# Performance work log

Hardware: AMD Instinct MI355X
Metric: run time of the kernel (lower is better)

The kernel has to match this reference:

```python
import jax, jax.numpy as jnp
import numpy as np
import math
from jax import lax

VOCAB = 32000
D = 128          # embedding_dim
S = 512          # seq_len == input_channels
B = 8
HID = 512        # hidden_size
NBUCK = 32       # n_buckets
NHYP = 5         # log2(n_buckets)
ENCODERS = 2
OUT = 6
EPS = 1e-5


def _positional_encoding(max_len, d):
    pos = np.arange(max_len, dtype=np.float32)[:, None]
    div = np.exp(np.arange(0, d, 2, dtype=np.float32) * (-math.log(10000.0) / d))
    pe = np.zeros((max_len, d), dtype=np.float32)
    pe[:, 0::2] = np.sin(pos * div)
    pe[:, 1::2] = np.cos(pos * div)
    return jnp.asarray(pe)


def setup_inputs() -> dict:
    key = jax.random.key(0)
    ks = jax.random.split(key, 10)
    emb = jax.random.normal(ks[0], (VOCAB, D), jnp.float32)
    emb = emb.at[VOCAB - 1].set(0.0)  # padding_idx row is zero in torch
    sc = 0.05
    return {
        "inputs": jax.random.randint(ks[1], (B, S), 0, VOCAB - 1),
        "emb": emb,
        # Faithful quirk: pe is indexed by x.size(0)=batch, so only pe[:B] is used.
        "pe": _positional_encoding(B, D),               # [B, D]
        "hyperplanes": jax.random.normal(ks[2], (D + 1, NHYP), jnp.float32),
        "Wq": jax.random.normal(ks[3], (D, D), jnp.float32) * sc,
        "bq": jnp.zeros((D,), jnp.float32),
        "Wv": jax.random.normal(ks[4], (D, D), jnp.float32) * sc,
        "bv": jnp.zeros((D,), jnp.float32),
        "ln_g": jnp.ones((D,), jnp.float32),
        "ln_b": jnp.zeros((D,), jnp.float32),
        "W1": jax.random.normal(ks[5], (D, HID), jnp.float32) * sc,
        "b1": jnp.zeros((HID,), jnp.float32),
        "W2": jax.random.normal(ks[6], (HID, D), jnp.float32) * sc,
        "b2": jnp.zeros((D,), jnp.float32),
        "Wm": jax.random.normal(ks[7], (S * D, OUT), jnp.float32) * 0.01,
        "bm": jnp.zeros((OUT,), jnp.float32),
    }


def _layernorm(x, g, b):
    mu = jnp.mean(x, axis=-1, keepdims=True)
    var = jnp.mean(jnp.square(x - mu), axis=-1, keepdims=True)
    return (x - mu) * lax.rsqrt(var + EPS) * g + b


def _lsh_attention(x, Wq, bq, Wv, bv, hyperplanes):
    q = x @ Wq + bq                                      # [B,S,D]
    v = x @ Wv + bv                                      # [B,S,D]
    # LSH bucket ids from q (hard threshold -> no grad through buckets)
    qh = jnp.concatenate([q, jnp.ones(q.shape[:-1] + (1,), q.dtype)], axis=-1)
    proj = jnp.einsum('bse,en->bsn', qh, hyperplanes)    # [B,S,NHYP]
    bits = (proj >= 0).astype(jnp.float32)
    pow2 = 2.0 ** jnp.arange(NHYP, dtype=jnp.float32)
    buckets = jnp.einsum('bsn,n->bs', bits, pow2).astype(jnp.int32)  # [B,S]
    scale = 1.0 / math.sqrt(D)

    def step(acc, i):
        # Faithful quirk: masked_fill zeros tokens IN bucket i (inverted mask).
        keep = (buckets != i)[..., None]                 # [B,S,1]
        qb = jnp.where(keep, q, 0.0)
        vb = jnp.where(keep, v, 0.0)
        att = jax.nn.softmax(jnp.einsum('bsd,btd->bst', qb, qb) * scale, axis=-1)
        return acc + jnp.einsum('bst,btd->bsd', att, vb), None

    out, _ = lax.scan(step, jnp.zeros_like(x), jnp.arange(NBUCK))
    return out


def reference(inputs, emb, pe, hyperplanes, Wq, bq, Wv, bv, ln_g, ln_b,
              W1, b1, W2, b2, Wm, bm):
    x = emb[inputs]                                      # [B,S,D]
    x = x + pe[:, None, :]                               # broadcast over seq (faithful quirk)
    for _ in range(ENCODERS):
        a = _lsh_attention(x, Wq, bq, Wv, bv, hyperplanes)
        x = _layernorm(a, ln_g, ln_b)
        x = (jax.nn.relu(x @ W1 + b1) @ W2 + b2) + x     # fc residual (dropout=eval)
        x = _layernorm(x, ln_g, ln_b)
    x = x.reshape(x.shape[0], -1)                        # [B, S*D]
    return x @ Wm + bm                                   # [B, OUT]
```

## Files before the change

kernel.cpp:

```cpp
#include <hip/hip_runtime.h>
#include <hip/hip_bf16.h>

#define BB   8
#define SS   512
#define DD   128
#define HH   512
#define NBK  32


__global__ void k_embed(const int* __restrict__ idx, const float* __restrict__ emb,
                        const float* __restrict__ pe, float* __restrict__ x) {
    int b = blockIdx.x;
    int t = b * 16384 + blockIdx.y * 256 + threadIdx.x;
    int tok = t >> 5, d4 = (t & 31) * 4;
    float4 ev = *(const float4*)&emb[(size_t)idx[tok] * DD + d4];
    float4 pv = *(const float4*)&pe[b * DD + d4];
    ev.x += pv.x; ev.y += pv.y; ev.z += pv.z; ev.w += pv.w;
    *(float4*)&x[(size_t)tok * DD + d4] = ev;
}

__global__ __launch_bounds__(256) void k_qvb(const float* __restrict__ x,
        const float* __restrict__ Wq, const float* __restrict__ bq,
        const float* __restrict__ Wv, const float* __restrict__ bv,
        const float* __restrict__ hyp,
        float* __restrict__ q, float* __restrict__ v, float* __restrict__ qT,
        int* __restrict__ bucket) {
    int rb = blockIdx.x * 32 + blockIdx.y;
    __shared__ __align__(16) float xs[16][132];
    __shared__ float qts[128][17];
    int tid = threadIdx.x;
    #pragma unroll
    for (int it = 0; it < 2; ++it) {
        int lin = tid + 256 * it;
        int r = lin >> 5, kq = (lin & 31) * 4;
        *(float4*)&xs[r][kq] = *(const float4*)&x[(size_t)(rb * 16 + r) * DD + kq];
    }
    __syncthreads();
    int tx = tid & 63;
    int ty = tid >> 6;
    float2 aq[4], av[4];
    #pragma unroll
    for (int i = 0; i < 4; ++i) { aq[i] = make_float2(0.f, 0.f); av[i] = make_float2(0.f, 0.f); }
    for (int g = 0; g < 32; ++g) {
        int kb = g * 4;
        float4 a0 = *(const float4*)&xs[ty * 4 + 0][kb];
        float4 a1 = *(const float4*)&xs[ty * 4 + 1][kb];
        float4 a2 = *(const float4*)&xs[ty * 4 + 2][kb];
        float4 a3 = *(const float4*)&xs[ty * 4 + 3][kb];
        #pragma unroll
        for (int j = 0; j < 4; ++j) {
            float2 wq = *(const float2*)&Wq[(size_t)(kb + j) * DD + tx * 2];
            float2 wv = *(const float2*)&Wv[(size_t)(kb + j) * DD + tx * 2];
            float c0 = (j == 0) ? a0.x : (j == 1) ? a0.y : (j == 2) ? a0.z : a0.w;
            float c1 = (j == 0) ? a1.x : (j == 1) ? a1.y : (j == 2) ? a1.z : a1.w;
            float c2 = (j == 0) ? a2.x : (j == 1) ? a2.y : (j == 2) ? a2.z : a2.w;
            float c3 = (j == 0) ? a3.x : (j == 1) ? a3.y : (j == 2) ? a3.z : a3.w;
            aq[0].x += c0 * wq.x; aq[0].y += c0 * wq.y; av[0].x += c0 * wv.x; av[0].y += c0 * wv.y;
            aq[1].x += c1 * wq.x; aq[1].y += c1 * wq.y; av[1].x += c1 * wv.x; av[1].y += c1 * wv.y;
            aq[2].x += c2 * wq.x; aq[2].y += c2 * wq.y; av[2].x += c2 * wv.x; av[2].y += c2 * wv.y;
            aq[3].x += c3 * wq.x; aq[3].y += c3 * wq.y; av[3].x += c3 * wv.x; av[3].y += c3 * wv.y;
        }
    }
    float2 bqv = *(const float2*)&bq[tx * 2];
    float2 bvv = *(const float2*)&bv[tx * 2];
    float2 oq[4], ov[4];
    #pragma unroll
    for (int i = 0; i < 4; ++i) {
        oq[i] = make_float2(aq[i].x + bqv.x, aq[i].y + bqv.y);
        ov[i] = make_float2(av[i].x + bvv.x, av[i].y + bvv.y);
        int row = rb * 16 + ty * 4 + i;
        *(float2*)&q[(size_t)row * DD + tx * 2] = oq[i];
        *(float2*)&v[(size_t)row * DD + tx * 2] = ov[i];
        qts[2 * tx][ty * 4 + i]     = oq[i].x;
        qts[2 * tx + 1][ty * 4 + i] = oq[i].y;
    }
    float h0[5], h1[5];
    #pragma unroll
    for (int h = 0; h < 5; ++h) {
        h0[h] = hyp[(2 * tx) * 5 + h];
        h1[h] = hyp[(2 * tx + 1) * 5 + h];
    }
    float pr[4][5];
    #pragma unroll
    for (int r = 0; r < 4; ++r)
        #pragma unroll
        for (int h = 0; h < 5; ++h)
            pr[r][h] = oq[r].x * h0[h] + oq[r].y * h1[h];
    #pragma unroll
    for (int o = 1; o < 64; o <<= 1)
        #pragma unroll
        for (int r = 0; r < 4; ++r)
            #pragma unroll
            for (int h = 0; h < 5; ++h)
                pr[r][h] += __shfl_xor(pr[r][h], o, 64);
    if (tx == 0) {
        #pragma unroll
        for (int r = 0; r < 4; ++r) {
            int bb = 0;
            #pragma unroll
            for (int h = 0; h < 5; ++h)
                if (pr[r][h] + hyp[128 * 5 + h] >= 0.f) bb |= (1 << h);
            bucket[rb * 16 + ty * 4 + r] = bb;
        }
    }
    __syncthreads();
    {
        int b  = blockIdx.x;
        int t0 = blockIdx.y * 16;
        int k  = tid >> 1, o = (tid & 1) * 8;
        float4 v0 = make_float4(qts[k][o], qts[k][o + 1], qts[k][o + 2], qts[k][o + 3]);
        float4 v1 = make_float4(qts[k][o + 4], qts[k][o + 5], qts[k][o + 6], qts[k][o + 7]);
        size_t base = ((size_t)b * DD + k) * SS + t0 + o;
        *(float4*)&qT[base]     = v0;
        *(float4*)&qT[base + 4] = v1;
    }
}

__global__ __launch_bounds__(256) void k_vb(const float* __restrict__ v,
        const int* __restrict__ bucket, float* __restrict__ Vb,
        int* __restrict__ cnt) {
    int b  = blockIdx.x;
    int bk = blockIdx.y;
    int tid = threadIdx.x;
    __shared__ int bkt_sh[512];
    __shared__ float red[128];
    bkt_sh[tid]       = bucket[b * SS + tid];
    bkt_sh[tid + 256] = bucket[b * SS + tid + 256];
    __syncthreads();
    int d = tid & 127, half = tid >> 7;
    const float* vbp = v + (size_t)b * SS * DD + d;
    float acc = 0.f;
    #pragma unroll 8
    for (int i = 0; i < 256; ++i) {
        int tok = half * 256 + i;
        float val = vbp[(size_t)tok * DD];
        acc += (bkt_sh[tok] == bk) ? val : 0.f;
    }
    if (half == 1) red[d] = acc;
    __syncthreads();
    if (half == 0)
        Vb[(size_t)((b << 5) + bk) * DD + d] = acc + red[d];
    if (tid < 64) {
        int c = 0;
        #pragma unroll
        for (int i = 0; i < 8; ++i) c += (bkt_sh[tid * 8 + i] == bk) ? 1 : 0;
        #pragma unroll
        for (int o = 1; o < 64; o <<= 1) c += __shfl_xor(c, o, 64);
        if (tid == 0) cnt[(b << 5) + bk] = c;
    }
}

__global__ __launch_bounds__(512) void k_gattn(const float* __restrict__ qT,
        const float* __restrict__ q, const float* __restrict__ v,
        const int* __restrict__ bucket, const int* __restrict__ cnt,
        const float* __restrict__ Vb,
        const float* __restrict__ g, const float* __restrict__ lb,
        float* __restrict__ x) {
    int bz = blockIdx.x, s0 = blockIdx.y * 16;
    int tid = threadIdx.x;
    __shared__ __align__(16) float qs[16][132];
    __shared__ __align__(16) float cs[16][528];
    __shared__ __align__(16) float osh[16][132];
    __shared__ int   bkt[512];
    __shared__ float Wsh[16][32];
    __shared__ float rsh[16][32];
    __shared__ float Zsh[16], Rsh[16], Msh[16];
    __shared__ float cntf[32];
    __shared__ int   bssh[16];
    {
        int r = tid >> 5, kq = (tid & 31) * 4;
        *(float4*)&qs[r][kq] = *(const float4*)&q[(size_t)(bz * SS + s0 + r) * DD + kq];
    }
    bkt[tid] = bucket[bz * SS + tid];
    if (tid < 32) cntf[tid] = (float)cnt[(bz << 5) + tid];
    if (tid < 16) bssh[tid] = bucket[bz * SS + s0 + tid];
    Wsh[tid >> 5][tid & 31] = 0.f;
    __syncthreads();
    const float scale = 0.088388347648318447f;
    {
        int kh   = tid >> 8;
        int rg   = (tid >> 7) & 1;
        int slot = tid & 127;
        float4 acc[8];
        #pragma unroll
        for (int i = 0; i < 8; ++i) acc[i] = make_float4(0.f, 0.f, 0.f, 0.f);
        const float* qtb = qT + (size_t)bz * DD * SS + (size_t)kh * 64 * SS + slot * 4;
        for (int gg = 0; gg < 16; ++gg) {
            int kb = kh * 64 + gg * 4;
            float4 a[8];
            #pragma unroll
            for (int i = 0; i < 8; ++i) a[i] = *(const float4*)&qs[rg * 8 + i][kb];
            #pragma unroll
            for (int j = 0; j < 4; ++j) {
                float4 b4 = *(const float4*)&qtb[(size_t)(gg * 4 + j) * SS];
                #pragma unroll
                for (int i = 0; i < 8; ++i) {
                    float c = (j == 0) ? a[i].x : (j == 1) ? a[i].y : (j == 2) ? a[i].z : a[i].w;
                    acc[i].x += c * b4.x; acc[i].y += c * b4.y;
                    acc[i].z += c * b4.z; acc[i].w += c * b4.w;
                }
            }
        }
        if (kh == 1) {
            #pragma unroll
            for (int i = 0; i < 8; ++i)
                *(float4*)&cs[rg * 8 + i][slot * 4] = acc[i];
        }
        __syncthreads();
        if (kh == 0) {
            #pragma unroll
            for (int i = 0; i < 8; ++i) {
                float4 p = *(const float4*)&cs[rg * 8 + i][slot * 4];
                p.x = (p.x + acc[i].x) * scale;
                p.y = (p.y + acc[i].y) * scale;
                p.z = (p.z + acc[i].z) * scale;
                p.w = (p.w + acc[i].w) * scale;
                *(float4*)&cs[rg * 8 + i][slot * 4] = p;
            }
        }
        __syncthreads();
    }
    int row = tid >> 5, l = tid & 31;
    {
        float m = 0.f;
        #pragma unroll
        for (int i = 0; i < 16; ++i) m = fmaxf(m, cs[row][l + 32 * i]);
        #pragma unroll
        for (int o = 1; o < 32; o <<= 1) m = fmaxf(m, __shfl_xor(m, o, 32));
        if (l == 0) Msh[row] = m;
    }
    __syncthreads();
    {
        float Ms = Msh[row];
        #pragma unroll
        for (int i = 0; i < 16; ++i) {
            int c = l + 32 * i;
            float ev = __expf(cs[row][c] - Ms);
            cs[row][c] = ev;
            atomicAdd(&Wsh[row][bkt[c]], ev);
        }
    }
    __syncthreads();
    if (tid < 16) {
        float z = 0.f;
        #pragma unroll
        for (int i = 0; i < NBK; ++i) z += Wsh[tid][i];
        Zsh[tid] = z;
    }
    __syncthreads();
    rsh[row][l] = 1.0f / (Zsh[row] - Wsh[row][l] + cntf[l] * __expf(-Msh[row]));
    __syncthreads();
    if (tid < 16) {
        int bs = bssh[tid];
        float R = 0.f;
        #pragma unroll
        for (int i = 0; i < NBK; ++i) R += (i == bs) ? 0.f : rsh[tid][i];
        Rsh[tid] = R;
    }
    __syncthreads();
    {
        float R = Rsh[row];
        int bs = bssh[row];
        #pragma unroll
        for (int i = 0; i < 16; ++i) {
            int c = l + 32 * i;
            int bc = bkt[c];
            float rsel = (bc == bs) ? 0.f : rsh[row][bc];
            cs[row][c] *= (R - rsel);
        }
    }
    __syncthreads();
    {
        int kh = tid >> 7;
        int rg = (tid >> 6) & 1;
        int cp = tid & 63;
        float2 acc[8];
        #pragma unroll
        for (int i = 0; i < 8; ++i) acc[i] = make_float2(0.f, 0.f);
        const float* vb_base = v + (size_t)bz * SS * DD + cp * 2;
        for (int gg = 0; gg < 32; ++gg) {
            int kb = kh * 128 + gg * 4;
            float4 a[8];
            #pragma unroll
            for (int i = 0; i < 8; ++i) a[i] = *(const float4*)&cs[rg * 8 + i][kb];
            #pragma unroll
            for (int j = 0; j < 4; ++j) {
                float2 v2 = *(const float2*)&vb_base[(size_t)(kb + j) * DD];
                #pragma unroll
                for (int i = 0; i < 8; ++i) {
                    float c = (j == 0) ? a[i].x : (j == 1) ? a[i].y : (j == 2) ? a[i].z : a[i].w;
                    acc[i].x += c * v2.x; acc[i].y += c * v2.y;
                }
            }
        }
        if (kh == 3) {
            #pragma unroll
            for (int i = 0; i < 8; ++i)
                *(float2*)&osh[rg * 8 + i][cp * 2] = acc[i];
        }
        __syncthreads();
        #pragma unroll
        for (int p = 2; p >= 1; --p) {
            if (kh == p) {
                #pragma unroll
                for (int i = 0; i < 8; ++i) {
                    float2 o = *(const float2*)&osh[rg * 8 + i][cp * 2];
                    o.x += acc[i].x; o.y += acc[i].y;
                    *(float2*)&osh[rg * 8 + i][cp * 2] = o;
                }
            }
            __syncthreads();
        }
        if (kh == 0) {
            float2 vs = make_float2(0.f, 0.f);
            #pragma unroll
            for (int i = 0; i < NBK; ++i) {
                float2 t = *(const float2*)&Vb[(size_t)((bz << 5) + i) * DD + cp * 2];
                vs.x += t.x; vs.y += t.y;
            }
            const float inv512 = 1.0f / 512.0f;
            #pragma unroll
            for (int i = 0; i < 8; ++i) {
                int r = rg * 8 + i;
                int bs = bssh[r];
                float2 vb2 = *(const float2*)&Vb[(size_t)((bz << 5) + bs) * DD + cp * 2];
                float2 p = *(const float2*)&osh[r][cp * 2];
                p.x += acc[i].x + (vs.x - vb2.x) * inv512;
                p.y += acc[i].y + (vs.y - vb2.y) * inv512;
                *(float2*)&osh[r][cp * 2] = p;
            }
        }
        __syncthreads();
    }
    {
        float4 val = *(const float4*)&osh[row][l * 4];
        float s = val.x + val.y + val.z + val.w;
        float ss = val.x * val.x + val.y * val.y + val.z * val.z + val.w * val.w;
        #pragma unroll
        for (int o = 1; o < 32; o <<= 1) {
            s  += __shfl_xor(s, o, 32);
            ss += __shfl_xor(ss, o, 32);
        }
        float mean = s * (1.f / 128.f);
        float var = ss * (1.f / 128.f) - mean * mean;
        float rstd = rsqrtf(var + 1e-5f);
        float4 gv = *(const float4*)&g[l * 4];
        float4 bv = *(const float4*)&lb[l * 4];
        float4 out;
        out.x = (val.x - mean) * rstd * gv.x + bv.x;
        out.y = (val.y - mean) * rstd * gv.y + bv.y;
        out.z = (val.z - mean) * rstd * gv.z + bv.z;
        out.w = (val.w - mean) * rstd * gv.w + bv.w;
        *(float4*)&x[(size_t)(bz * SS + s0 + row) * DD + l * 4] = out;
    }
}

__global__ __launch_bounds__(512) void k_ffn(const float* __restrict__ x,
        const float* __restrict__ W1, const float* __restrict__ b1,
        const float* __restrict__ W2, const float* __restrict__ b2,
        const float* __restrict__ g, const float* __restrict__ lb,
        float* __restrict__ xout) {
    int rb = blockIdx.x * 32 + blockIdx.y;
    int tid = threadIdx.x;
    __shared__ __align__(16) float xs[16][132];
    __shared__ __align__(16) float hs[16][520];
    __shared__ __align__(16) float osh[16][132];
    {
        int r = tid >> 5, kq = (tid & 31) * 4;
        *(float4*)&xs[r][kq] = *(const float4*)&x[(size_t)(rb * 16 + r) * DD + kq];
    }
    __syncthreads();
    {
        int kh   = tid >> 8;
        int rg   = (tid >> 7) & 1;
        int slot = tid & 127;
        float4 acc[8];
        #pragma unroll
        for (int i = 0; i < 8; ++i) acc[i] = make_float4(0.f, 0.f, 0.f, 0.f);
        for (int gg = 0; gg < 16; ++gg) {
            int kb = kh * 64 + gg * 4;
            float4 a[8];
            #pragma unroll
            for (int i = 0; i < 8; ++i) a[i] = *(const float4*)&xs[rg * 8 + i][kb];
            #pragma unroll
            for (int j = 0; j < 4; ++j) {
                float4 w = *(const float4*)&W1[(size_t)(kb + j) * HH + slot * 4];
                #pragma unroll
                for (int i = 0; i < 8; ++i) {
                    float c = (j == 0) ? a[i].x : (j == 1) ? a[i].y : (j == 2) ? a[i].z : a[i].w;
                    acc[i].x += c * w.x; acc[i].y += c * w.y;
                    acc[i].z += c * w.z; acc[i].w += c * w.w;
                }
            }
        }
        if (kh == 1) {
            #pragma unroll
            for (int i = 0; i < 8; ++i)
                *(float4*)&hs[rg * 8 + i][slot * 4] = acc[i];
        }
        __syncthreads();
        if (kh == 0) {
            float4 bi = *(const float4*)&b1[slot * 4];
            #pragma unroll
            for (int i = 0; i < 8; ++i) {
                float4 p = *(const float4*)&hs[rg * 8 + i][slot * 4];
                p.x = fmaxf(p.x + acc[i].x + bi.x, 0.f);
                p.y = fmaxf(p.y + acc[i].y + bi.y, 0.f);
                p.z = fmaxf(p.z + acc[i].z + bi.z, 0.f);
                p.w = fmaxf(p.w + acc[i].w + bi.w, 0.f);
                *(float4*)&hs[rg * 8 + i][slot * 4] = p;
            }
        }
        __syncthreads();
    }
    {
        int kh = tid >> 7;
        int rg = (tid >> 6) & 1;
        int cp = tid & 63;
        float2 acc[8];
        #pragma unroll
        for (int i = 0; i < 8; ++i) acc[i] = make_float2(0.f, 0.f);
        for (int gg = 0; gg < 32; ++gg) {
            int kb = kh * 128 + gg * 4;
            float4 a[8];
            #pragma unroll
            for (int i = 0; i < 8; ++i) a[i] = *(const float4*)&hs[rg * 8 + i][kb];
            #pragma unroll
            for (int j = 0; j < 4; ++j) {
                float2 w2 = *(const float2*)&W2[(size_t)(kb + j) * DD + cp * 2];
                #pragma unroll
                for (int i = 0; i < 8; ++i) {
                    float c = (j == 0) ? a[i].x : (j == 1) ? a[i].y : (j == 2) ? a[i].z : a[i].w;
                    acc[i].x += c * w2.x; acc[i].y += c * w2.y;
                }
            }
        }
        if (kh == 3) {
            #pragma unroll
            for (int i = 0; i < 8; ++i)
                *(float2*)&osh[rg * 8 + i][cp * 2] = acc[i];
        }
        __syncthreads();
        #pragma unroll
        for (int p = 2; p >= 1; --p) {
            if (kh == p) {
                #pragma unroll
                for (int i = 0; i < 8; ++i) {
                    float2 o = *(const float2*)&osh[rg * 8 + i][cp * 2];
                    o.x += acc[i].x; o.y += acc[i].y;
                    *(float2*)&osh[rg * 8 + i][cp * 2] = o;
                }
            }
            __syncthreads();
        }
        if (kh == 0) {
            float2 bi = *(const float2*)&b2[cp * 2];
            #pragma unroll
            for (int i = 0; i < 8; ++i) {
                int r = rg * 8 + i;
                float2 res = *(const float2*)&xs[r][cp * 2];
                float2 p = *(const float2*)&osh[r][cp * 2];
                p.x += acc[i].x + bi.x + res.x;
                p.y += acc[i].y + bi.y + res.y;
                *(float2*)&osh[r][cp * 2] = p;
            }
        }
        __syncthreads();
    }
    int row = tid >> 5, l = tid & 31;
    float4 val = *(const float4*)&osh[row][l * 4];
    float s = val.x + val.y + val.z + val.w;
    float ss = val.x * val.x + val.y * val.y + val.z * val.z + val.w * val.w;
    #pragma unroll
    for (int o = 1; o < 32; o <<= 1) {
        s  += __shfl_xor(s, o, 32);
        ss += __shfl_xor(ss, o, 32);
    }
    float mean = s * (1.f / 128.f);
    float var = ss * (1.f / 128.f) - mean * mean;
    float rstd = rsqrtf(var + 1e-5f);
    float4 gv = *(const float4*)&g[l * 4];
    float4 bv = *(const float4*)&lb[l * 4];
    float4 out;
    out.x = (val.x - mean) * rstd * gv.x + bv.x;
    out.y = (val.y - mean) * rstd * gv.y + bv.y;
    out.z = (val.z - mean) * rstd * gv.z + bv.z;
    out.w = (val.w - mean) * rstd * gv.w + bv.w;
    *(float4*)&xout[(size_t)(rb * 16 + row) * DD + l * 4] = out;
}

__global__ __launch_bounds__(256) void k_final(const float* __restrict__ x,
        const float* __restrict__ Wm, const float* __restrict__ bm,
        float* __restrict__ out) {
    int b = blockIdx.x >> 5, chunk = blockIdx.x & 31;
    int tid = threadIdx.x;
    const float* xr = x + (size_t)b * 65536 + chunk * 2048;
    const float* wr = Wm + (size_t)(chunk * 2048) * 6;
    float p[6] = {0.f, 0.f, 0.f, 0.f, 0.f, 0.f};
    #pragma unroll
    for (int it = 0; it < 8; ++it) {
        int j = tid + 256 * it;
        float xv = xr[j];
        const float* w = wr + (size_t)j * 6;
        p[0] += xv * w[0]; p[1] += xv * w[1]; p[2] += xv * w[2];
        p[3] += xv * w[3]; p[4] += xv * w[4]; p[5] += xv * w[5];
    }
    #pragma unroll
    for (int o = 0; o < 6; ++o)
        #pragma unroll
        for (int off = 1; off < 64; off <<= 1)
            p[o] += __shfl_xor(p[o], off, 64);
    __shared__ float red[4][6];
    int wv = tid >> 6;
    if ((tid & 63) == 0)
        #pragma unroll
        for (int o = 0; o < 6; ++o) red[wv][o] = p[o];
    __syncthreads();
    if (tid < 6) {
        float sv = red[0][tid] + red[1][tid] + red[2][tid] + red[3][tid];
        if (chunk == 0) sv += bm[tid];
        atomicAdd(&out[b * 6 + tid], sv);
    }
}

extern "C" void kernel_launch(void* const* d_in, const int* in_sizes, int n_in,
                              void* d_out, int out_size, void* d_ws, size_t ws_size,
                              hipStream_t stream) {
    const int*   inputs = (const int*)  d_in[0];
    const float* emb    = (const float*)d_in[1];
    const float* pe     = (const float*)d_in[2];
    const float* hyp    = (const float*)d_in[3];
    const float* Wq     = (const float*)d_in[4];
    const float* bq     = (const float*)d_in[5];
    const float* Wv     = (const float*)d_in[6];
    const float* bv     = (const float*)d_in[7];
    const float* ln_g   = (const float*)d_in[8];
    const float* ln_b   = (const float*)d_in[9];
    const float* W1     = (const float*)d_in[10];
    const float* b1     = (const float*)d_in[11];
    const float* W2     = (const float*)d_in[12];
    const float* b2     = (const float*)d_in[13];
    const float* Wm     = (const float*)d_in[14];
    const float* bm     = (const float*)d_in[15];

    float* F = (float*)d_ws;
    float* x     = F + 0;
    float* q     = F + 524288;
    float* v     = F + 1048576;
    float* qT    = F + 1572864;
    float* Vb    = F + 2097152;
    int*   cnt   = (int*)(F + 2129920);
    int*   bucket= (int*)(F + 2130176);

    hipMemsetAsync(d_out, 0, (size_t)out_size * 4, stream);
    k_embed<<<dim3(8, 64), 256, 0, stream>>>(inputs, emb, pe, x);

    for (int enc = 0; enc < 2; ++enc) {
        k_qvb<<<dim3(8, 32), 256, 0, stream>>>(x, Wq, bq, Wv, bv, hyp, q, v, qT, bucket);
        k_vb<<<dim3(8, 32), 256, 0, stream>>>(v, bucket, Vb, cnt);
        k_gattn<<<dim3(8, 32), 512, 0, stream>>>(qT, q, v, bucket, cnt, Vb, ln_g, ln_b, x);
        k_ffn<<<dim3(8, 32), 512, 0, stream>>>(x, W1, b1, W2, b2, ln_g, ln_b, x);
    }
    k_final<<<48 * 32 / 6, 256, 0, stream>>>(x, Wm, bm, (float*)d_out);
}
```

Before: 249.0 us.

## Fuse attention-output layernorm with FFN into one encoder kernel

Merges the attention kernel with the FFN kernel, so the layer-normed attention output stays in shared memory (reusing qs/cs buffers) and is not written to and re-read from global memory between launches. This also removes one launch per encoder. The attention-value and W2 stages switch from 8-row float2 tiles to 4-row float4 tiles, and the final projection kernel now uses float4 loads on x and Wm. The risk is that the fused kernel's larger register and shared-memory footprint lowers occupancy in the attention stage.

After: 251.7 us. About the same (+1.1%).

```diff
diff --git a/kernel.cpp b/kernel.cpp
--- a/kernel.cpp
+++ b/kernel.cpp
@@ -150,11 +150,13 @@
     }
 }
 
-__global__ __launch_bounds__(512) void k_gattn(const float* __restrict__ qT,
+__global__ __launch_bounds__(512) void k_enc(const float* __restrict__ qT,
         const float* __restrict__ q, const float* __restrict__ v,
         const int* __restrict__ bucket, const int* __restrict__ cnt,
         const float* __restrict__ Vb,
         const float* __restrict__ g, const float* __restrict__ lb,
+        const float* __restrict__ W1, const float* __restrict__ b1,
+        const float* __restrict__ W2, const float* __restrict__ b2,
         float* __restrict__ x) {
     int bz = blockIdx.x, s0 = blockIdx.y * 16;
     int tid = threadIdx.x;
@@ -272,62 +274,187 @@
     __syncthreads();
     {
         int kh = tid >> 7;
-        int rg = (tid >> 6) & 1;
-        int cp = tid & 63;
-        float2 acc[8];
-        #pragma unroll
-        for (int i = 0; i < 8; ++i) acc[i] = make_float2(0.f, 0.f);
-        const float* vb_base = v + (size_t)bz * SS * DD + cp * 2;
+        int rg = (tid >> 5) & 3;
+        int cp = tid & 31;
+        float4 acc[4];
+        #pragma unroll
+        for (int i = 0; i < 4; ++i) acc[i] = make_float4(0.f, 0.f, 0.f, 0.f);
+        const float* vb_base = v + (size_t)bz * SS * DD + cp * 4;
         for (int gg = 0; gg < 32; ++gg) {
             int kb = kh * 128 + gg * 4;
+            float4 a[4];
+            #pragma unroll
+            for (int i = 0; i < 4; ++i) a[i] = *(const float4*)&cs[rg * 4 + i][kb];
+            #pragma unroll
+            for (int j = 0; j < 4; ++j) {
+                float4 vj = *(const float4*)&vb_base[(size_t)(kb + j) * DD];
+                #pragma unroll
+                for (int i = 0; i < 4; ++i) {
+                    float c = (j == 0) ? a[i].x : (j == 1) ? a[i].y : (j == 2) ? a[i].z : a[i].w;
+                    acc[i].x += c * vj.x; acc[i].y += c * vj.y;
+                    acc[i].z += c * vj.z; acc[i].w += c * vj.w;
+                }
+            }
+        }
+        if (kh == 3) {
+            #pragma unroll
+            for (int i = 0; i < 4; ++i)
+                *(float4*)&osh[rg * 4 + i][cp * 4] = acc[i];
+        }
+        __syncthreads();
+        #pragma unroll
+        for (int p = 2; p >= 1; --p) {
+            if (kh == p) {
+                #pragma unroll
+                for (int i = 0; i < 4; ++i) {
+                    float4 o = *(const float4*)&osh[rg * 4 + i][cp * 4];
+                    o.x += acc[i].x; o.y += acc[i].y; o.z += acc[i].z; o.w += acc[i].w;
+                    *(float4*)&osh[rg * 4 + i][cp * 4] = o;
+                }
+            }
+            __syncthreads();
+        }
+        if (kh == 0) {
+            float4 vs = make_float4(0.f, 0.f, 0.f, 0.f);
+            #pragma unroll
+            for (int i = 0; i < NBK; ++i) {
+                float4 t = *(const float4*)&Vb[(size_t)((bz << 5) + i) * DD + cp * 4];
+                vs.x += t.x; vs.y += t.y; vs.z += t.z; vs.w += t.w;
+            }
+            const float inv512 = 1.0f / 512.0f;
+            #pragma unroll
+            for (int i = 0; i < 4; ++i) {
+                int r = rg * 4 + i;
+                int bs = bssh[r];
+                float4 vb4 = *(const float4*)&Vb[(size_t)((bz << 5) + bs) * DD + cp * 4];
+                float4 p = *(const float4*)&osh[r][cp * 4];
+                p.x += acc[i].x + (vs.x - vb4.x) * inv512;
+                p.y += acc[i].y + (vs.y - vb4.y) * inv512;
+                p.z += acc[i].z + (vs.z - vb4.z) * inv512;
+                p.w += acc[i].w + (vs.w - vb4.w) * inv512;
+                *(float4*)&osh[r][cp * 4] = p;
+            }
+        }
+        __syncthreads();
+    }
+    {
+        float4 val = *(const float4*)&osh[row][l * 4];
+        float s = val.x + val.y + val.z + val.w;
+        float ss = val.x * val.x + val.y * val.y + val.z * val.z + val.w * val.w;
+        #pragma unroll
+        for (int o = 1; o < 32; o <<= 1) {
+            s  += __shfl_xor(s, o, 32);
+            ss += __shfl_xor(ss, o, 32);
+        }
+        float mean = s * (1.f / 128.f);
+        float var = ss * (1.f / 128.f) - mean * mean;
+        float rstd = rsqrtf(var + 1e-5f);
+        float4 gv = *(const float4*)&g[l * 4];
+        float4 bv = *(const float4*)&lb[l * 4];
+        float4 out;
+        out.x = (val.x - mean) * rstd * gv.x + bv.x;
+        out.y = (val.y - mean) * rstd * gv.y + bv.y;
+        out.z = (val.z - mean) * rstd * gv.z + bv.z;
+        out.w = (val.w - mean) * rstd * gv.w + bv.w;
+        *(float4*)&qs[row][l * 4] = out;
+    }
+    __syncthreads();
+    {
+        int kh   = tid >> 8;
+        int rg   = (tid >> 7) & 1;
+        int slot = tid & 127;
+        float4 acc[8];
+        #pragma unroll
+        for (int i = 0; i < 8; ++i) acc[i] = make_float4(0.f, 0.f, 0.f, 0.f);
+        for (int gg = 0; gg < 16; ++gg) {
+            int kb = kh * 64 + gg * 4;
             float4 a[8];
             #pragma unroll
-            for (int i = 0; i < 8; ++i) a[i] = *(const float4*)&cs[rg * 8 + i][kb];
+            for (int i = 0; i < 8; ++i) a[i] = *(const float4*)&qs[rg * 8 + i][kb];
             #pragma unroll
             for (int j = 0; j < 4; ++j) {
-                float2 v2 = *(const float2*)&vb_base[(size_t)(kb + j) * DD];
+                float4 w = *(const float4*)&W1[(size_t)(kb + j) * HH + slot * 4];
                 #pragma unroll
                 for (int i = 0; i < 8; ++i) {
                     float c = (j == 0) ? a[i].x : (j == 1) ? a[i].y : (j == 2) ? a[i].z : a[i].w;
-                    acc[i].x += c * v2.x; acc[i].y += c * v2.y;
+                    acc[i].x += c * w.x; acc[i].y += c * w.y;
+                    acc[i].z += c * w.z; acc[i].w += c * w.w;
                 }
             }
         }
+        if (kh == 1) {
+            #pragma unroll
+            for (int i = 0; i < 8; ++i)
+                *(float4*)&cs[rg * 8 + i][slot * 4] = acc[i];
+        }
+        __syncthreads();
+        if (kh == 0) {
+            float4 bi = *(const float4*)&b1[slot * 4];
+            #pragma unroll
+            for (int i = 0; i < 8; ++i) {
+                float4 p = *(const float4*)&cs[rg * 8 + i][slot * 4];
+                p.x = fmaxf(p.x + acc[i].x + bi.x, 0.f);
+                p.y = fmaxf(p.y + acc[i].y + bi.y, 0.f);
+                p.z = fmaxf(p.z + acc[i].z + bi.z, 0.f);
+                p.w = fmaxf(p.w + acc[i].w + bi.w, 0.f);
+                *(float4*)&cs[rg * 8 + i][slot * 4] = p;
+            }
+        }
+        __syncthreads();
+    }
+    {
+        int kh = tid >> 7;
+        int rg = (tid >> 5) & 3;
+        int cp = tid & 31;
+        float4 acc[4];
+        #pragma unroll
+        for (int i = 0; i < 4; ++i) acc[i] = make_float4(0.f, 0.f, 0.f, 0.f);
+        for (int gg = 0; gg < 32; ++gg) {
+            int kb = kh * 128 + gg * 4;
+            float4 a[4];
+            #pragma unroll
+            for (int i = 0; i < 4; ++i) a[i] = *(const float4*)&cs[rg * 4 + i][kb];
+            #pragma unroll
+            for (int j = 0; j < 4; ++j) {
+                float4 w = *(const float4*)&W2[(size_t)(kb + j) * DD + cp * 4];
+                #pragma unroll
+                for (int i = 0; i < 4; ++i) {
+                    float c = (j == 0) ? a[i].x : (j == 1) ? a[i].y : (j == 2) ? a[i].z : a[i].w;
+                    acc[i].x += c * w.x; acc[i].y += c * w.y;
+                    acc[i].z += c * w.z; acc[i].w += c * w.w;
+                }
+            }
+        }
         if (kh == 3) {
             #pragma unroll
-            for (int i = 0; i < 8; ++i)
-                *(float2*)&osh[rg * 8 + i][cp * 2] = acc[i];
+            for (int i = 0; i < 4; ++i)
+                *(float4*)&osh[rg * 4 + i][cp * 4] = acc[i];
         }
         __syncthreads();
         #pragma unroll
         for (int p = 2; p >= 1; --p) {
             if (kh == p) {
                 #pragma unroll
-                for (int i = 0; i < 8; ++i) {
-                    float2 o = *(const float2*)&osh[rg * 8 + i][cp * 2];
-                    o.x += acc[i].x; o.y += acc[i].y;
-                    *(float2*)&osh[rg * 8 + i][cp * 2] = o;
+                for (int i = 0; i < 4; ++i) {
+                    float4 o = *(const float4*)&osh[rg * 4 + i][cp * 4];
+                    o.x += acc[i].x; o.y += acc[i].y; o.z += acc[i].z; o.w += acc[i].w;
+                    *(float4*)&osh[rg * 4 + i][cp * 4] = o;
                 }
             }
             __syncthreads();
         }
         if (kh == 0) {
-            float2 vs = make_float2(0.f, 0.f);
-            #pragma unroll
-            for (int i = 0; i < NBK; ++i) {
-                float2 t = *(const float2*)&Vb[(size_t)((bz << 5) + i) * DD + cp * 2];
-                vs.x += t.x; vs.y += t.y;
-            }
-            const float inv512 = 1.0f / 512.0f;
-            #pragma unroll
-            for (int i = 0; i < 8; ++i) {
-                int r = rg * 8 + i;
-                int bs = bssh[r];
-                float2 vb2 = *(const float2*)&Vb[(size_t)((bz << 5) + bs) * DD + cp * 2];
-                float2 p = *(const float2*)&osh[r][cp * 2];
-                p.x += acc[i].x + (vs.x - vb2.x) * inv512;
-                p.y += acc[i].y + (vs.y - vb2.y) * inv512;
-                *(float2*)&osh[r][cp * 2] = p;
+            float4 bi = *(const float4*)&b2[cp * 4];
+            #pragma unroll
+            for (int i = 0; i < 4; ++i) {
+                int r = rg * 4 + i;
+                float4 res = *(const float4*)&qs[r][cp * 4];
+                float4 p = *(const float4*)&osh[r][cp * 4];
+                p.x += acc[i].x + bi.x + res.x;
+                p.y += acc[i].y + bi.y + res.y;
+                p.z += acc[i].z + bi.z + res.z;
+                p.w += acc[i].w + bi.w + res.w;
+                *(float4*)&osh[r][cp * 4] = p;
             }
         }
         __syncthreads();
@@ -355,155 +482,31 @@
     }
 }
 
-__global__ __launch_bounds__(512) void k_ffn(const float* __restrict__ x,
-        const float* __restrict__ W1, const float* __restrict__ b1,
-        const float* __restrict__ W2, const float* __restrict__ b2,
-        const float* __restrict__ g, const float* __restrict__ lb,
-        float* __restrict__ xout) {
-    int rb = blockIdx.x * 32 + blockIdx.y;
-    int tid = threadIdx.x;
-    __shared__ __align__(16) float xs[16][132];
-    __shared__ __align__(16) float hs[16][520];
-    __shared__ __align__(16) float osh[16][132];
-    {
-        int r = tid >> 5, kq = (tid & 31) * 4;
-        *(float4*)&xs[r][kq] = *(const float4*)&x[(size_t)(rb * 16 + r) * DD + kq];
-    }
-    __syncthreads();
-    {
-        int kh   = tid >> 8;
-        int rg   = (tid >> 7) & 1;
-        int slot = tid & 127;
-        float4 acc[8];
-        #pragma unroll
-        for (int i = 0; i < 8; ++i) acc[i] = make_float4(0.f, 0.f, 0.f, 0.f);
-        for (int gg = 0; gg < 16; ++gg) {
-            int kb = kh * 64 + gg * 4;
-            float4 a[8];
-            #pragma unroll
-            for (int i = 0; i < 8; ++i) a[i] = *(const float4*)&xs[rg * 8 + i][kb];
-            #pragma unroll
-            for (int j = 0; j < 4; ++j) {
-                float4 w = *(const float4*)&W1[(size_t)(kb + j) * HH + slot * 4];
-                #pragma unroll
-                for (int i = 0; i < 8; ++i) {
-                    float c = (j == 0) ? a[i].x : (j == 1) ? a[i].y : (j == 2) ? a[i].z : a[i].w;
-                    acc[i].x += c * w.x; acc[i].y += c * w.y;
-                    acc[i].z += c * w.z; acc[i].w += c * w.w;
-                }
-            }
-        }
-        if (kh == 1) {
-            #pragma unroll
-            for (int i = 0; i < 8; ++i)
-                *(float4*)&hs[rg * 8 + i][slot * 4] = acc[i];
-        }
-        __syncthreads();
-        if (kh == 0) {
-            float4 bi = *(const float4*)&b1[slot * 4];
-            #pragma unroll
-            for (int i = 0; i < 8; ++i) {
-                float4 p = *(const float4*)&hs[rg * 8 + i][slot * 4];
-                p.x = fmaxf(p.x + acc[i].x + bi.x, 0.f);
-                p.y = fmaxf(p.y + acc[i].y + bi.y, 0.f);
-                p.z = fmaxf(p.z + acc[i].z + bi.z, 0.f);
-                p.w = fmaxf(p.w + acc[i].w + bi.w, 0.f);
-                *(float4*)&hs[rg * 8 + i][slot * 4] = p;
-            }
-        }
-        __syncthreads();
-    }
-    {
-        int kh = tid >> 7;
-        int rg = (tid >> 6) & 1;
-        int cp = tid & 63;
-        float2 acc[8];
-        #pragma unroll
-        for (int i = 0; i < 8; ++i) acc[i] = make_float2(0.f, 0.f);
-        for (int gg = 0; gg < 32; ++gg) {
-            int kb = kh * 128 + gg * 4;
-            float4 a[8];
-            #pragma unroll
-            for (int i = 0; i < 8; ++i) a[i] = *(const float4*)&hs[rg * 8 + i][kb];
-            #pragma unroll
-            for (int j = 0; j < 4; ++j) {
-                float2 w2 = *(const float2*)&W2[(size_t)(kb + j) * DD + cp * 2];
-                #pragma unroll
-                for (int i = 0; i < 8; ++i) {
-                    float c = (j == 0) ? a[i].x : (j == 1) ? a[i].y : (j == 2) ? a[i].z : a[i].w;
-                    acc[i].x += c * w2.x; acc[i].y += c * w2.y;
-                }
-            }
-        }
-        if (kh == 3) {
-            #pragma unroll
-            for (int i = 0; i < 8; ++i)
-                *(float2*)&osh[rg * 8 + i][cp * 2] = acc[i];
-        }
-        __syncthreads();
-        #pragma unroll
-        for (int p = 2; p >= 1; --p) {
-            if (kh == p) {
-                #pragma unroll
-                for (int i = 0; i < 8; ++i) {
-                    float2 o = *(const float2*)&osh[rg * 8 + i][cp * 2];
-                    o.x += acc[i].x; o.y += acc[i].y;
-                    *(float2*)&osh[rg * 8 + i][cp * 2] = o;
-                }
-            }
-            __syncthreads();
-        }
-        if (kh == 0) {
-            float2 bi = *(const float2*)&b2[cp * 2];
-            #pragma unroll
-            for (int i = 0; i < 8; ++i) {
-                int r = rg * 8 + i;
-                float2 res = *(const float2*)&xs[r][cp * 2];
-                float2 p = *(const float2*)&osh[r][cp * 2];
-                p.x += acc[i].x + bi.x + res.x;
-                p.y += acc[i].y + bi.y + res.y;
-                *(float2*)&osh[r][cp * 2] = p;
-            }
-        }
-        __syncthreads();
-    }
-    int row = tid >> 5, l = tid & 31;
-    float4 val = *(const float4*)&osh[row][l * 4];
-    float s = val.x + val.y + val.z + val.w;
-    float ss = val.x * val.x + val.y * val.y + val.z * val.z + val.w * val.w;
-    #pragma unroll
-    for (int o = 1; o < 32; o <<= 1) {
-        s  += __shfl_xor(s, o, 32);
-        ss += __shfl_xor(ss, o, 32);
-    }
-    float mean = s * (1.f / 128.f);
-    float var = ss * (1.f / 128.f) - mean * mean;
-    float rstd = rsqrtf(var + 1e-5f);
-    float4 gv = *(const float4*)&g[l * 4];
-    float4 bv = *(const float4*)&lb[l * 4];
-    float4 out;
-    out.x = (val.x - mean) * rstd * gv.x + bv.x;
-    out.y = (val.y - mean) * rstd * gv.y + bv.y;
-    out.z = (val.z - mean) * rstd * gv.z + bv.z;
-    out.w = (val.w - mean) * rstd * gv.w + bv.w;
-    *(float4*)&xout[(size_t)(rb * 16 + row) * DD + l * 4] = out;
-}
-
 __global__ __launch_bounds__(256) void k_final(const float* __restrict__ x,
         const float* __restrict__ Wm, const float* __restrict__ bm,
         float* __restrict__ out) {
-    int b = blockIdx.x >> 5, chunk = blockIdx.x & 31;
+    int b = blockIdx.x, chunk = blockIdx.y;
     int tid = threadIdx.x;
     const float* xr = x + (size_t)b * 65536 + chunk * 2048;
     const float* wr = Wm + (size_t)(chunk * 2048) * 6;
     float p[6] = {0.f, 0.f, 0.f, 0.f, 0.f, 0.f};
     #pragma unroll
-    for (int it = 0; it < 8; ++it) {
-        int j = tid + 256 * it;
-        float xv = xr[j];
+    for (int it = 0; it < 2; ++it) {
+        int j = (tid + 256 * it) * 4;
+        float4 xv = *(const float4*)&xr[j];
         const float* w = wr + (size_t)j * 6;
-        p[0] += xv * w[0]; p[1] += xv * w[1]; p[2] += xv * w[2];
-        p[3] += xv * w[3]; p[4] += xv * w[4]; p[5] += xv * w[5];
+        float4 w0 = *(const float4*)&w[0];
+        float4 w1 = *(const float4*)&w[4];
+        float4 w2 = *(const float4*)&w[8];
+        float4 w3 = *(const float4*)&w[12];
+        float4 w4 = *(const float4*)&w[16];
+        float4 w5 = *(const float4*)&w[20];
+        p[0] += xv.x * w0.x + xv.y * w1.z + xv.z * w3.x + xv.w * w4.z;
+        p[1] += xv.x * w0.y + xv.y * w1.w + xv.z * w3.y + xv.w * w4.w;
+        p[2] += xv.x * w0.z + xv.y * w2.x + xv.z * w3.z + xv.w * w5.x;
+        p[3] += xv.x * w0.w + xv.y * w2.y + xv.z * w3.w + xv.w * w5.y;
+        p[4] += xv.x * w1.x + xv.y * w2.z + xv.z * w4.x + xv.w * w5.z;
+        p[5] += xv.x * w1.y + xv.y * w2.w + xv.z * w4.y + xv.w * w5.w;
     }
     #pragma unroll
     for (int o = 0; o < 6; ++o)
@@ -558,8 +561,8 @@
     for (int enc = 0; enc < 2; ++enc) {
         k_qvb<<<dim3(8, 32), 256, 0, stream>>>(x, Wq, bq, Wv, bv, hyp, q, v, qT, bucket);
         k_vb<<<dim3(8, 32), 256, 0, stream>>>(v, bucket, Vb, cnt);
-        k_gattn<<<dim3(8, 32), 512, 0, stream>>>(qT, q, v, bucket, cnt, Vb, ln_g, ln_b, x);
-        k_ffn<<<dim3(8, 32), 512, 0, stream>>>(x, W1, b1, W2, b2, ln_g, ln_b, x);
-    }
-    k_final<<<48 * 32 / 6, 256, 0, stream>>>(x, Wm, bm, (float*)d_out);
+        k_enc<<<dim3(8, 32), 512, 0, stream>>>(qT, q, v, bucket, cnt, Vb,
+                                               ln_g, ln_b, W1, b1, W2, b2, x);
+    }
+    k_final<<<dim3(8, 32), 256, 0, stream>>>(x, Wm, bm, (float*)d_out);
 }
```
